# Kernel optimization log

Hardware: AMD Instinct MI355X
Metric: run time of the kernel (lower is better)

Reference implementation:

```python
import jax, jax.numpy as jnp
import numpy as np

T, B, IN, HID = 512, 64, 1024, 1024

def _linear_params(key, fan_in, fan_out):
    kw, kb = jax.random.split(key)
    bound = 1.0 / np.sqrt(fan_in)
    W = jax.random.uniform(kw, (fan_out, fan_in), jnp.float32, -bound, bound)
    b = jax.random.uniform(kb, (fan_out,), jnp.float32, -bound, bound)
    return W, b

def setup_inputs() -> dict:
    key = jax.random.key(0)
    ks = jax.random.split(key, 9)
    inp = {
        'inputs': jax.random.normal(ks[0], (T, B, IN), jnp.float32),
        'H0': jnp.zeros((B, HID), jnp.float32),
        'C0': jnp.zeros((B, HID), jnp.float32),
    }
    names = [('Wix','bix'),('Wih','bih'),('Wfx','bfx'),('Wfh','bfh'),
             ('Wox','box'),('Woh','boh'),('Wcx','bcx'),('Wch','bch')]
    fan_ins = [IN, HID, IN, HID, IN, HID, IN, HID]
    for (wn, bn), fi, k in zip(names, fan_ins, ks[1:]):
        W, b = _linear_params(k, fi, HID)
        inp[wn] = W
        inp[bn] = b
    return inp

def _lstm(inputs, H0, C0, Wix, bix, Wih, bih, Wfx, bfx, Wfh, bfh,
          Wox, box, Woh, boh, Wcx, bcx, Wch, bch):
    # Stack gate weights: order i, f, o, c_tilde
    Wx = jnp.concatenate([Wix, Wfx, Wox, Wcx], axis=0)      # [4H, IN]
    Wh = jnp.concatenate([Wih, Wfh, Woh, Wch], axis=0)      # [4H, H]
    bias = jnp.concatenate([bix + bih, bfx + bfh, box + boh, bcx + bch])  # [4H]
    # Precompute all input projections in one big GEMM: [T,B,4H]
    xproj = jnp.einsum('tbi,gi->tbg', inputs, Wx) + bias
    H = HID

    def step(carry, xg):
        h, c = carry
        g = xg + h @ Wh.T                                    # [B,4H]
        i = jax.nn.sigmoid(g[:, 0*H:1*H])
        f = jax.nn.sigmoid(g[:, 1*H:2*H])
        o = jax.nn.sigmoid(g[:, 2*H:3*H])
        ct = jnp.tanh(g[:, 3*H:4*H])
        c = f * c + i * ct
        h = o * jnp.tanh(c)
        return (h, c), h

    (Hf, Cf), outs = jax.lax.scan(step, (H0, C0), xproj)
    return outs, Hf, Cf

def reference(inputs, H0, C0, Wix, bix, Wih, bih, Wfx, bfx, Wfh, bfh,
              Wox, box, Woh, boh, Wcx, bcx, Wch, bch):
    return _lstm(inputs, H0, C0, Wix, bix, Wih, bih, Wfx, bfx, Wfh, bfh,
                 Wox, box, Woh, boh, Wcx, bcx, Wch, bch)
```

## Files before the change

### kernel.cpp

```cpp
#include <hip/hip_runtime.h>
#include <hip/hip_bf16.h>
#include <math.h>

#define T_STEPS 512
#define BATCH   64
#define INDIM   1024
#define HDIM    1024
#define NWG     128
#define NPROD   128
#define HSLOT   16384
#define XGSLOT  262144

using bf16x8 = __attribute__((ext_vector_type(8))) __bf16;
using f32x4  = __attribute__((ext_vector_type(4))) float;
typedef unsigned long long u64;

struct WP {
    const float* wx[4];
    const float* wh[4];
    const float* bx[4];
    const float* bh[4];
};

__global__ void pack_weights(WP p, __hip_bfloat16* __restrict__ Wx,
                             __hip_bfloat16* __restrict__ Wh, float* __restrict__ bias)
{
    int i = blockIdx.x * blockDim.x + threadIdx.x;
    const int stride = gridDim.x * blockDim.x;
    const int total = 4 * HDIM * INDIM;
    for (int idx = i; idx < total; idx += stride) {
        int g = idx >> 20;
        int r = idx & ((1 << 20) - 1);
        Wx[idx] = __float2bfloat16(p.wx[g][r]);
        Wh[idx] = __float2bfloat16(p.wh[g][r]);
    }
    if (i < 4 * HDIM) {
        int g = i >> 10, r = i & 1023;
        bias[i] = p.bx[g][r] + p.bh[g][r];
    }
}

__global__ void cast_pack(const float* __restrict__ in, u64* __restrict__ xbp)
{
    const int total = T_STEPS * BATCH * (INDIM / 8);
    int i = blockIdx.x * blockDim.x + threadIdx.x;
    const int stride = gridDim.x * blockDim.x;
    for (; i < total; i += stride) {
        const int t  = i >> 13;
        const int r  = i & 8191;
        const int b  = r >> 7;
        const int j  = (r & 127) << 3;
        const float* src = in + ((size_t)t << 16) + (b << 10) + j;
        float4 v0 = *reinterpret_cast<const float4*>(src);
        float4 v1 = *reinterpret_cast<const float4*>(src + 4);
        union { __hip_bfloat16 bh[8]; u64 q[2]; } u;
        u.bh[0] = __float2bfloat16(v0.x); u.bh[1] = __float2bfloat16(v0.y);
        u.bh[2] = __float2bfloat16(v0.z); u.bh[3] = __float2bfloat16(v0.w);
        u.bh[4] = __float2bfloat16(v1.x); u.bh[5] = __float2bfloat16(v1.y);
        u.bh[6] = __float2bfloat16(v1.z); u.bh[7] = __float2bfloat16(v1.w);
        const int wv = j >> 8, kk = (j >> 5) & 7, lhi = (j >> 3) & 3;
        const int m = b >> 4, rA = b & 15;
        const int lane = (lhi << 4) + rA;
        const int blk  = (((wv << 3) + kk) << 2) + m;
        u64* d = xbp + ((size_t)t << 14) + (size_t)blk * 128 + (lane << 1);
        d[0] = u.q[0];
        d[1] = u.q[1];
    }
}

__global__ void init_state(const float* __restrict__ H0, const float* __restrict__ C0,
                           __hip_bfloat16* __restrict__ hx, float* __restrict__ c)
{
    int i = blockIdx.x * blockDim.x + threadIdx.x;
    if (i < BATCH * HDIM) {
        int b = i >> 10, j = i & 1023;
        int m = b >> 4, rA = b & 15;
        int wv = j >> 8, kk = (j >> 5) & 7, lhi = (j >> 3) & 3, ii = j & 7;
        size_t idx = ((((size_t)(wv << 3) + kk) << 2) + m) * 512
                   + (((lhi << 4) + rA) << 3) + ii;
        hx[idx] = __float2bfloat16(H0[i]);
        c[i] = C0[i];
    }
}

__global__ void epilogue(const float* __restrict__ lasth, const float* __restrict__ c,
                         float* __restrict__ Hf, float* __restrict__ Cf)
{
    int i = blockIdx.x * blockDim.x + threadIdx.x;
    if (i < BATCH * HDIM) {
        Hf[i] = lasth[i];
        Cf[i] = c[i];
    }
}

__device__ __forceinline__ float fast_sigmoid(float x)
{
    return 1.f / (1.f + __expf(-x));
}
__device__ __forceinline__ float fast_tanh(float x)
{
    x = fminf(15.f, fmaxf(-15.f, x));
    const float e = __expf(2.f * x);
    return (e - 1.f) / (e + 1.f);
}

__global__ __launch_bounds__(256, 1) void lstm_persist(
    const u64* __restrict__ xbp,
    const __hip_bfloat16* __restrict__ Wx,
    const __hip_bfloat16* __restrict__ Wh,
    const float* __restrict__ bias,
    u64* __restrict__ hx,
    float* __restrict__ cbuf,
    float* __restrict__ out,
    unsigned* __restrict__ hflags,
    unsigned* __restrict__ xflags,
    float* __restrict__ xg)
{
    __shared__ float gl[4][64][33];
    __shared__ float hs[64][9];

    const int tid  = threadIdx.x;
    const int w    = tid >> 6;
    const int lane = tid & 63;
    const int rA   = lane & 15;
    const int kg   = (lane >> 4) << 3;
    const int bw   = blockIdx.x;

    if (bw >= NWG) {
        const int p   = bw - NWG;
        const int grp = p >> 5;
        const int pn  = p & 31;
        const int nb0 = pn << 7;

        for (int s = grp; s < T_STEPS; s += 4) {
            u64 aq[8][4][2];
#pragma unroll
            for (int kk = 0; kk < 8; ++kk)
#pragma unroll
                for (int m = 0; m < 4; ++m) {
                    const u64* q = xbp + ((size_t)s << 14)
                                 + ((((size_t)(w << 3) + kk) << 2) + m) * 128
                                 + (lane << 1);
                    aq[kk][m][0] = q[0];
                    aq[kk][m][1] = q[1];
                }

            if (s >= 8) {
                const unsigned need = (unsigned)(s - 7);
                const unsigned* f0 = hflags + lane * 16;
                const unsigned* f1 = hflags + (lane + 64) * 16;
                int guard = 1 << 18;
                while (--guard > 0) {
                    int ok = (__hip_atomic_load(f0, __ATOMIC_RELAXED, __HIP_MEMORY_SCOPE_AGENT) >= need) &&
                             (__hip_atomic_load(f1, __ATOMIC_RELAXED, __HIP_MEMORY_SCOPE_AGENT) >= need);
                    if (__all(ok)) break;
                    __builtin_amdgcn_s_sleep(1);
                }
            }

            float* xgs = xg + (size_t)(s & 7) * XGSLOT;
#pragma unroll 1
            for (int g32 = 0; g32 < 4; ++g32) {
                const int nb = nb0 + (g32 << 5);
                bf16x8 wxf[2][8];
#pragma unroll
                for (int n2 = 0; n2 < 2; ++n2) {
                    const __hip_bfloat16* xr =
                        Wx + (size_t)(nb + (n2 << 4) + rA) * 1024 + (w << 8) + kg;
#pragma unroll
                    for (int kk = 0; kk < 8; ++kk)
                        wxf[n2][kk] = *reinterpret_cast<const bf16x8*>(xr + (kk << 5));
                }
                f32x4 acc[2][4] = {};
#pragma unroll
                for (int kk = 0; kk < 8; ++kk)
#pragma unroll
                    for (int m = 0; m < 4; ++m) {
                        union { u64 q[2]; bf16x8 v; } c;
                        c.q[0] = aq[kk][m][0];
                        c.q[1] = aq[kk][m][1];
#pragma unroll
                        for (int n2 = 0; n2 < 2; ++n2)
                            acc[n2][m] = __builtin_amdgcn_mfma_f32_16x16x32_bf16(
                                c.v, wxf[n2][kk], acc[n2][m], 0, 0, 0);
                    }
#pragma unroll
                for (int n2 = 0; n2 < 2; ++n2)
#pragma unroll
                    for (int m = 0; m < 4; ++m) {
                        const int bb = (m << 4) + ((lane >> 4) << 2);
#pragma unroll
                        for (int r = 0; r < 4; ++r)
                            gl[w][bb + r][(n2 << 4) + rA] = acc[n2][m][r];
                    }
                __syncthreads();
                {
                    const int np = tid >> 3;
                    const int bb = (tid & 7) << 3;
                    union { float f[8]; u64 q[4]; } v;
#pragma unroll
                    for (int i = 0; i < 8; ++i)
                        v.f[i] = gl[0][bb + i][np] + gl[1][bb + i][np]
                               + gl[2][bb + i][np] + gl[3][bb + i][np];
                    u64* d = (u64*)(xgs + (size_t)(nb + np) * 64 + bb);
#pragma unroll
                    for (int q4 = 0; q4 < 4; ++q4)
                        __hip_atomic_store(d + q4, v.q[q4],
                                           __ATOMIC_RELAXED, __HIP_MEMORY_SCOPE_AGENT);
                }
                __syncthreads();
            }
            if (tid == 0)
                __hip_atomic_store(&xflags[p * 16], (unsigned)(s + 1),
                                   __ATOMIC_RELAXED, __HIP_MEMORY_SCOPE_AGENT);
        }
        return;
    }

    const int j0 = bw << 3;

    bf16x8 whf[2][8];
#pragma unroll
    for (int n2 = 0; n2 < 2; ++n2) {
        const int row  = (n2 << 4) + rA;
        const int grow = ((row >> 3) << 10) + j0 + (row & 7);
        const __hip_bfloat16* wr = Wh + ((size_t)grow << 10) + (w << 8) + kg;
#pragma unroll
        for (int kk = 0; kk < 8; ++kk)
            whf[n2][kk] = *reinterpret_cast<const bf16x8*>(wr + (kk << 5));
    }

    const int b = lane;
    float creg[2], brg[2][4];
#pragma unroll
    for (int e = 0; e < 2; ++e) {
        const int cl = (w << 1) + e;
        creg[e] = cbuf[(b << 10) + j0 + cl];
#pragma unroll
        for (int g = 0; g < 4; ++g) brg[e][g] = bias[(g << 10) + j0 + cl];
    }

    const int pblk = (((bw >> 5) << 3) + ((bw >> 2) & 7)) << 2;
    const unsigned gsto = (unsigned)(pblk + (b >> 4)) * 256
                        + (unsigned)((((bw & 3) << 4) + (b & 15)) << 2) + w;
    const unsigned* fq = hflags + (((w << 5) + (lane & 31)) << 4);

#define XV_FETCH(dst, ss)                                                      \
    do {                                                                       \
        const unsigned* fx_ = xflags +                                         \
            (((((unsigned)(ss) & 3) << 5) + (bw >> 4) + ((lane & 3) << 3)) << 4); \
        int guard_ = 1 << 18;                                                  \
        while (--guard_ > 0) {                                                 \
            unsigned v_ = __hip_atomic_load(fx_, __ATOMIC_RELAXED, __HIP_MEMORY_SCOPE_AGENT); \
            int ok_ = (lane < 4) ? (int)(v_ >= (unsigned)(ss) + 1) : 1;        \
            if (__all(ok_)) break;                                             \
            __builtin_amdgcn_s_sleep(1);                                       \
        }                                                                      \
        const float* xgs_ = xg + (size_t)((ss) & 7) * XGSLOT;                  \
        _Pragma("unroll") for (int e = 0; e < 2; ++e)                          \
        _Pragma("unroll") for (int g = 0; g < 4; ++g) {                        \
            unsigned uv_ = __hip_atomic_load(                                  \
                (const unsigned*)(xgs_ +                                       \
                    (size_t)((g << 10) + j0 + (w << 1) + e) * 64 + b),         \
                __ATOMIC_RELAXED, __HIP_MEMORY_SCOPE_AGENT);                   \
            dst[e][g] = __uint_as_float(uv_);                                  \
        }                                                                      \
    } while (0)

    float xv[2][4];
    XV_FETCH(xv, 0);

    for (int s = 0; s < T_STEPS; ++s) {
        const unsigned t = (unsigned)s;
        const u64* hp = hx + (size_t)(t & 3) * HSLOT;
        u64*       hn = hx + (size_t)((t + 1) & 3) * HSLOT;

        {
            int guard = 1 << 18;
            while (--guard > 0) {
                unsigned v = __hip_atomic_load(fq, __ATOMIC_RELAXED, __HIP_MEMORY_SCOPE_AGENT);
                if (__all((int)(v >= t))) break;
                __builtin_amdgcn_s_sleep(1);
            }
        }

        f32x4 acc[2][4] = {};
        {
            u64 aq[8][4][2];
#pragma unroll
            for (int kk = 0; kk < 8; ++kk)
#pragma unroll
                for (int m = 0; m < 4; ++m) {
                    const u64* q = hp + ((((size_t)(w << 3) + kk) << 2) + m) * 128
                                     + (lane << 1);
                    aq[kk][m][0] = __hip_atomic_load(q,     __ATOMIC_RELAXED, __HIP_MEMORY_SCOPE_AGENT);
                    aq[kk][m][1] = __hip_atomic_load(q + 1, __ATOMIC_RELAXED, __HIP_MEMORY_SCOPE_AGENT);
                }
            __builtin_amdgcn_sched_barrier(0);
#pragma unroll
            for (int kk = 0; kk < 8; ++kk)
#pragma unroll
                for (int m = 0; m < 4; ++m) {
                    union { u64 q[2]; bf16x8 v; } c;
                    c.q[0] = aq[kk][m][0];
                    c.q[1] = aq[kk][m][1];
#pragma unroll
                    for (int n2 = 0; n2 < 2; ++n2)
                        acc[n2][m] = __builtin_amdgcn_mfma_f32_16x16x32_bf16(
                            c.v, whf[n2][kk], acc[n2][m], 0, 0, 0);
                }
        }

#pragma unroll
        for (int n2 = 0; n2 < 2; ++n2)
#pragma unroll
            for (int m = 0; m < 4; ++m) {
                const int bb = (m << 4) + ((lane >> 4) << 2);
#pragma unroll
                for (int r = 0; r < 4; ++r)
                    gl[w][bb + r][(n2 << 4) + rA] = acc[n2][m][r];
            }
        __syncthreads();

        {
            float hv[2];
#pragma unroll
            for (int e = 0; e < 2; ++e) {
                const int cl = (w << 1) + e;
                float gv[4];
#pragma unroll
                for (int g = 0; g < 4; ++g)
                    gv[g] = gl[0][b][(g << 3) + cl] + gl[1][b][(g << 3) + cl]
                          + gl[2][b][(g << 3) + cl] + gl[3][b][(g << 3) + cl]
                          + brg[e][g] + xv[e][g];
                const float i_ = fast_sigmoid(gv[0]);
                const float f_ = fast_sigmoid(gv[1]);
                const float o_ = fast_sigmoid(gv[2]);
                const float ct = fast_tanh(gv[3]);
                const float cn = f_ * creg[e] + i_ * ct;
                creg[e] = cn;
                hv[e] = o_ * fast_tanh(cn);
                hs[b][cl] = hv[e];
            }
            union { __hip_bfloat16 bh[2]; unsigned u; } pk;
            pk.bh[0] = __float2bfloat16(hv[0]);
            pk.bh[1] = __float2bfloat16(hv[1]);
            __hip_atomic_store((unsigned*)hn + gsto, pk.u,
                               __ATOMIC_RELAXED, __HIP_MEMORY_SCOPE_AGENT);
        }
        __syncthreads();

        if (tid == 0)
            __hip_atomic_store(&hflags[bw * 16], t + 1,
                               __ATOMIC_RELAXED, __HIP_MEMORY_SCOPE_AGENT);

        if (s + 1 < T_STEPS) XV_FETCH(xv, s + 1);

        if (tid < 64) {
            float v[8];
#pragma unroll
            for (int k = 0; k < 8; ++k) v[k] = hs[tid][k];
            float* orow = out + (((size_t)s << 6) + tid) * 1024 + j0;
            *reinterpret_cast<float4*>(orow)     = make_float4(v[0], v[1], v[2], v[3]);
            *reinterpret_cast<float4*>(orow + 4) = make_float4(v[4], v[5], v[6], v[7]);
        }
    }

#pragma unroll
    for (int e = 0; e < 2; ++e)
        cbuf[(b << 10) + j0 + (w << 1) + e] = creg[e];
}

extern "C" void kernel_launch(void* const* d_in, const int* in_sizes, int n_in,
                              void* d_out, int out_size, void* d_ws, size_t ws_size,
                              hipStream_t stream)
{
    const float* inputs = (const float*)d_in[0];
    const float* H0     = (const float*)d_in[1];
    const float* C0     = (const float*)d_in[2];

    WP wp;
    wp.wx[0] = (const float*)d_in[3];  wp.bx[0] = (const float*)d_in[4];
    wp.wh[0] = (const float*)d_in[5];  wp.bh[0] = (const float*)d_in[6];
    wp.wx[1] = (const float*)d_in[7];  wp.bx[1] = (const float*)d_in[8];
    wp.wh[1] = (const float*)d_in[9];  wp.bh[1] = (const float*)d_in[10];
    wp.wx[2] = (const float*)d_in[11]; wp.bx[2] = (const float*)d_in[12];
    wp.wh[2] = (const float*)d_in[13]; wp.bh[2] = (const float*)d_in[14];
    wp.wx[3] = (const float*)d_in[15]; wp.bx[3] = (const float*)d_in[16];
    wp.wh[3] = (const float*)d_in[17]; wp.bh[3] = (const float*)d_in[18];

    char* ws = (char*)d_ws;
    size_t off = 0;
    auto alloc = [&](size_t bytes) {
        void* p = ws + off;
        off = (off + bytes + 255) & ~(size_t)255;
        return p;
    };
    __hip_bfloat16* Wx    = (__hip_bfloat16*)alloc((size_t)4 * HDIM * INDIM * 2);
    __hip_bfloat16* Wh    = (__hip_bfloat16*)alloc((size_t)4 * HDIM * HDIM * 2);
    float*          bias  = (float*)alloc((size_t)4 * HDIM * 4);
    u64*            xbp   = (u64*)alloc((size_t)T_STEPS * HSLOT * 8);
    u64*            hx    = (u64*)alloc((size_t)4 * HSLOT * 8);
    float*          cbuf  = (float*)alloc((size_t)BATCH * HDIM * 4);
    unsigned*       hflags= (unsigned*)alloc((size_t)NWG * 16 * 4);
    unsigned*       xflags= (unsigned*)alloc((size_t)NPROD * 16 * 4);
    float*          xg    = (float*)alloc((size_t)8 * XGSLOT * 4);
    if (off > ws_size) return;

    float* out = (float*)d_out;

    hipMemsetAsync(hflags, 0, (size_t)NWG * 16 * 4, stream);
    hipMemsetAsync(xflags, 0, (size_t)NPROD * 16 * 4, stream);
    hipLaunchKernelGGL(pack_weights, dim3(2048), dim3(256), 0, stream, wp, Wx, Wh, bias);
    hipLaunchKernelGGL(cast_pack, dim3(4096), dim3(256), 0, stream, inputs, xbp);
    hipLaunchKernelGGL(init_state, dim3(256), dim3(256), 0, stream,
                       H0, C0, (__hip_bfloat16*)hx, cbuf);

    hipLaunchKernelGGL(lstm_persist, dim3(NWG + NPROD), dim3(256), 0, stream,
                       (const u64*)xbp, (const __hip_bfloat16*)Wx,
                       (const __hip_bfloat16*)Wh, (const float*)bias,
                       hx, cbuf, out, hflags, xflags, xg);

    hipLaunchKernelGGL(epilogue, dim3(256), dim3(256), 0, stream,
                       out + (size_t)(T_STEPS - 1) * BATCH * HDIM, cbuf,
                       out + (size_t)T_STEPS * BATCH * HDIM,
                       out + (size_t)T_STEPS * BATCH * HDIM + BATCH * HDIM);
}
```

Measured before the change: 2.331 ms.

## Split batch into two independent recurrence chains to overlap gate math with GEMM

The persistent LSTM kernel now splits the 64-row batch into two 32-row chains, each with its own h ring buffer and flag array. Within each step the chain-A GEMM and gates run, then A's flag is published, then chain B runs, so other workgroups can start chain A of the next step while B is still finishing. This targets the serialized cross-workgroup wait-GEMM-gate latency on the recurrent critical path. In exchange it adds an extra flag wait, extra syncthreads, and smaller MFMA batches per GEMM.

```diff
diff --git a/kernel.cpp b/kernel.cpp
--- a/kernel.cpp
+++ b/kernel.cpp
@@ -8,7 +8,7 @@
 #define HDIM    1024
 #define NWG     128
 #define NPROD   128
-#define HSLOT   16384
+#define HSLOT2  8192
 #define XGSLOT  262144
 
 using bf16x8 = __attribute__((ext_vector_type(8))) __bf16;
@@ -74,9 +74,11 @@
     int i = blockIdx.x * blockDim.x + threadIdx.x;
     if (i < BATCH * HDIM) {
         int b = i >> 10, j = i & 1023;
-        int m = b >> 4, rA = b & 15;
+        int chain = b >> 5, bc = b & 31;
+        int m = bc >> 4, rA = bc & 15;
         int wv = j >> 8, kk = (j >> 5) & 7, lhi = (j >> 3) & 3, ii = j & 7;
-        size_t idx = ((((size_t)(wv << 3) + kk) << 2) + m) * 512
+        size_t idx = (size_t)chain * 4 * HSLOT2 * 4
+                   + ((((size_t)(wv << 3) + kk) << 1) + m) * 512
                    + (((lhi << 4) + rA) << 3) + ii;
         hx[idx] = __float2bfloat16(H0[i]);
         c[i] = C0[i];
@@ -112,7 +114,8 @@
     u64* __restrict__ hx,
     float* __restrict__ cbuf,
     float* __restrict__ out,
-    unsigned* __restrict__ hflags,
+    unsigned* __restrict__ hflagsA,
+    unsigned* __restrict__ hflagsB,
     unsigned* __restrict__ xflags,
     float* __restrict__ xg)
 {
@@ -147,8 +150,8 @@
 
             if (s >= 8) {
                 const unsigned need = (unsigned)(s - 7);
-                const unsigned* f0 = hflags + lane * 16;
-                const unsigned* f1 = hflags + (lane + 64) * 16;
+                const unsigned* f0 = hflagsB + lane * 16;
+                const unsigned* f1 = hflagsB + (lane + 64) * 16;
                 int guard = 1 << 18;
                 while (--guard > 0) {
                     int ok = (__hip_atomic_load(f0, __ATOMIC_RELAXED, __HIP_MEMORY_SCOPE_AGENT) >= need) &&
@@ -240,10 +243,14 @@
         for (int g = 0; g < 4; ++g) brg[e][g] = bias[(g << 10) + j0 + cl];
     }
 
-    const int pblk = (((bw >> 5) << 3) + ((bw >> 2) & 7)) << 2;
-    const unsigned gsto = (unsigned)(pblk + (b >> 4)) * 256
-                        + (unsigned)((((bw & 3) << 4) + (b & 15)) << 2) + w;
-    const unsigned* fq = hflags + (((w << 5) + (lane & 31)) << 4);
+    const int bc    = lane & 31;
+    const int pblk2 = (((bw >> 5) << 3) + ((bw >> 2) & 7)) << 1;
+    const unsigned gsto = (unsigned)(pblk2 + (bc >> 4)) * 256
+                        + (unsigned)((((bw & 3) << 4) + (bc & 15)) << 2) + w;
+    const unsigned* fqA = hflagsA + (((w << 5) + (lane & 31)) << 4);
+    const unsigned* fqB = hflagsB + (((w << 5) + (lane & 31)) << 4);
+    u64* const hcA = hx;
+    u64* const hcB = hx + 4 * HSLOT2;
 
 #define XV_FETCH(dst, ss)                                                      \
     do {                                                                       \
@@ -267,94 +274,107 @@
         }                                                                      \
     } while (0)
 
+#define CHAIN_GEMM(fq, hbase, t, acc)                                          \
+    do {                                                                       \
+        int guard_ = 1 << 18;                                                  \
+        while (--guard_ > 0) {                                                 \
+            unsigned v_ = __hip_atomic_load(fq, __ATOMIC_RELAXED, __HIP_MEMORY_SCOPE_AGENT); \
+            if (__all((int)(v_ >= (t)))) break;                                \
+            __builtin_amdgcn_s_sleep(1);                                       \
+        }                                                                      \
+        const u64* hp_ = (hbase) + (size_t)((t) & 3) * HSLOT2;                 \
+        u64 aq_[8][2][2];                                                      \
+        _Pragma("unroll") for (int kk = 0; kk < 8; ++kk)                       \
+        _Pragma("unroll") for (int m = 0; m < 2; ++m) {                        \
+            const u64* q_ = hp_ + ((((size_t)(w << 3) + kk) << 1) + m) * 128   \
+                               + (lane << 1);                                  \
+            aq_[kk][m][0] = __hip_atomic_load(q_,     __ATOMIC_RELAXED, __HIP_MEMORY_SCOPE_AGENT); \
+            aq_[kk][m][1] = __hip_atomic_load(q_ + 1, __ATOMIC_RELAXED, __HIP_MEMORY_SCOPE_AGENT); \
+        }                                                                      \
+        __builtin_amdgcn_sched_barrier(0);                                     \
+        _Pragma("unroll") for (int kk = 0; kk < 8; ++kk)                       \
+        _Pragma("unroll") for (int m = 0; m < 2; ++m) {                        \
+            union { u64 q[2]; bf16x8 v; } c_;                                  \
+            c_.q[0] = aq_[kk][m][0];                                           \
+            c_.q[1] = aq_[kk][m][1];                                           \
+            _Pragma("unroll") for (int n2 = 0; n2 < 2; ++n2)                   \
+                acc[n2][m] = __builtin_amdgcn_mfma_f32_16x16x32_bf16(          \
+                    c_.v, whf[n2][kk], acc[n2][m], 0, 0, 0);                   \
+        }                                                                      \
+    } while (0)
+
+#define GL_WRITE(acc, base)                                                    \
+    do {                                                                       \
+        _Pragma("unroll") for (int n2 = 0; n2 < 2; ++n2)                       \
+        _Pragma("unroll") for (int m = 0; m < 2; ++m) {                        \
+            const int bb = (base) + (m << 4) + ((lane >> 4) << 2);             \
+            _Pragma("unroll") for (int r = 0; r < 4; ++r)                      \
+                gl[w][bb + r][(n2 << 4) + rA] = acc[n2][m][r];                 \
+        }                                                                      \
+    } while (0)
+
+#define GATES(lo, hnp)                                                         \
+    do {                                                                       \
+        if ((lane & 32) == (lo)) {                                             \
+            float hv_[2];                                                      \
+            _Pragma("unroll") for (int e = 0; e < 2; ++e) {                    \
+                const int cl = (w << 1) + e;                                   \
+                float gv_[4];                                                  \
+                _Pragma("unroll") for (int g = 0; g < 4; ++g)                  \
+                    gv_[g] = gl[0][b][(g << 3) + cl] + gl[1][b][(g << 3) + cl] \
+                           + gl[2][b][(g << 3) + cl] + gl[3][b][(g << 3) + cl] \
+                           + brg[e][g] + xv[e][g];                             \
+                const float i_ = fast_sigmoid(gv_[0]);                         \
+                const float f_ = fast_sigmoid(gv_[1]);                         \
+                const float o_ = fast_sigmoid(gv_[2]);                         \
+                const float ct_ = fast_tanh(gv_[3]);                           \
+                const float cn_ = f_ * creg[e] + i_ * ct_;                     \
+                creg[e] = cn_;                                                 \
+                hv_[e] = o_ * fast_tanh(cn_);                                  \
+                hs[b][cl] = hv_[e];                                            \
+            }                                                                  \
+            union { __hip_bfloat16 bh[2]; unsigned u; } pk_;                   \
+            pk_.bh[0] = __float2bfloat16(hv_[0]);                              \
+            pk_.bh[1] = __float2bfloat16(hv_[1]);                              \
+            __hip_atomic_store((unsigned*)(hnp) + gsto, pk_.u,                 \
+                               __ATOMIC_RELAXED, __HIP_MEMORY_SCOPE_AGENT);    \
+        }                                                                      \
+    } while (0)
+
+
     float xv[2][4];
     XV_FETCH(xv, 0);
 
     for (int s = 0; s < T_STEPS; ++s) {
         const unsigned t = (unsigned)s;
-        const u64* hp = hx + (size_t)(t & 3) * HSLOT;
-        u64*       hn = hx + (size_t)((t + 1) & 3) * HSLOT;
+        u64* hnA = hcA + (size_t)((t + 1) & 3) * HSLOT2;
+        u64* hnB = hcB + (size_t)((t + 1) & 3) * HSLOT2;
 
         {
-            int guard = 1 << 18;
-            while (--guard > 0) {
-                unsigned v = __hip_atomic_load(fq, __ATOMIC_RELAXED, __HIP_MEMORY_SCOPE_AGENT);
-                if (__all((int)(v >= t))) break;
-                __builtin_amdgcn_s_sleep(1);
-            }
-        }
-
-        f32x4 acc[2][4] = {};
-        {
-            u64 aq[8][4][2];
-#pragma unroll
-            for (int kk = 0; kk < 8; ++kk)
-#pragma unroll
-                for (int m = 0; m < 4; ++m) {
-                    const u64* q = hp + ((((size_t)(w << 3) + kk) << 2) + m) * 128
-                                     + (lane << 1);
-                    aq[kk][m][0] = __hip_atomic_load(q,     __ATOMIC_RELAXED, __HIP_MEMORY_SCOPE_AGENT);
-                    aq[kk][m][1] = __hip_atomic_load(q + 1, __ATOMIC_RELAXED, __HIP_MEMORY_SCOPE_AGENT);
-                }
-            __builtin_amdgcn_sched_barrier(0);
-#pragma unroll
-            for (int kk = 0; kk < 8; ++kk)
-#pragma unroll
-                for (int m = 0; m < 4; ++m) {
-                    union { u64 q[2]; bf16x8 v; } c;
-                    c.q[0] = aq[kk][m][0];
-                    c.q[1] = aq[kk][m][1];
-#pragma unroll
-                    for (int n2 = 0; n2 < 2; ++n2)
-                        acc[n2][m] = __builtin_amdgcn_mfma_f32_16x16x32_bf16(
-                            c.v, whf[n2][kk], acc[n2][m], 0, 0, 0);
-                }
-        }
-
-#pragma unroll
-        for (int n2 = 0; n2 < 2; ++n2)
-#pragma unroll
-            for (int m = 0; m < 4; ++m) {
-                const int bb = (m << 4) + ((lane >> 4) << 2);
-#pragma unroll
-                for (int r = 0; r < 4; ++r)
-                    gl[w][bb + r][(n2 << 4) + rA] = acc[n2][m][r];
-            }
-        __syncthreads();
-
-        {
-            float hv[2];
-#pragma unroll
-            for (int e = 0; e < 2; ++e) {
-                const int cl = (w << 1) + e;
-                float gv[4];
-#pragma unroll
-                for (int g = 0; g < 4; ++g)
-                    gv[g] = gl[0][b][(g << 3) + cl] + gl[1][b][(g << 3) + cl]
-                          + gl[2][b][(g << 3) + cl] + gl[3][b][(g << 3) + cl]
-                          + brg[e][g] + xv[e][g];
-                const float i_ = fast_sigmoid(gv[0]);
-                const float f_ = fast_sigmoid(gv[1]);
-                const float o_ = fast_sigmoid(gv[2]);
-                const float ct = fast_tanh(gv[3]);
-                const float cn = f_ * creg[e] + i_ * ct;
-                creg[e] = cn;
-                hv[e] = o_ * fast_tanh(cn);
-                hs[b][cl] = hv[e];
-            }
-            union { __hip_bfloat16 bh[2]; unsigned u; } pk;
-            pk.bh[0] = __float2bfloat16(hv[0]);
-            pk.bh[1] = __float2bfloat16(hv[1]);
-            __hip_atomic_store((unsigned*)hn + gsto, pk.u,
-                               __ATOMIC_RELAXED, __HIP_MEMORY_SCOPE_AGENT);
+            f32x4 accA[2][2] = {};
+            CHAIN_GEMM(fqA, hcA, t, accA);
+            GL_WRITE(accA, 0);
         }
         __syncthreads();
-
+        GATES(0, hnA);
+
+        {
+            f32x4 accB[2][2] = {};
+            CHAIN_GEMM(fqB, hcB, t, accB);
+            GL_WRITE(accB, 32);
+        }
+        __syncthreads();
         if (tid == 0)
-            __hip_atomic_store(&hflags[bw * 16], t + 1,
+            __hip_atomic_store(&hflagsA[bw * 16], t + 1,
                                __ATOMIC_RELAXED, __HIP_MEMORY_SCOPE_AGENT);
+        GATES(32, hnB);
 
         if (s + 1 < T_STEPS) XV_FETCH(xv, s + 1);
+
+        __syncthreads();
+        if (tid == 0)
+            __hip_atomic_store(&hflagsB[bw * 16], t + 1,
+                               __ATOMIC_RELAXED, __HIP_MEMORY_SCOPE_AGENT);
 
         if (tid < 64) {
             float v[8];
@@ -396,20 +416,22 @@
         off = (off + bytes + 255) & ~(size_t)255;
         return p;
     };
-    __hip_bfloat16* Wx    = (__hip_bfloat16*)alloc((size_t)4 * HDIM * INDIM * 2);
-    __hip_bfloat16* Wh    = (__hip_bfloat16*)alloc((size_t)4 * HDIM * HDIM * 2);
-    float*          bias  = (float*)alloc((size_t)4 * HDIM * 4);
-    u64*            xbp   = (u64*)alloc((size_t)T_STEPS * HSLOT * 8);
-    u64*            hx    = (u64*)alloc((size_t)4 * HSLOT * 8);
-    float*          cbuf  = (float*)alloc((size_t)BATCH * HDIM * 4);
-    unsigned*       hflags= (unsigned*)alloc((size_t)NWG * 16 * 4);
-    unsigned*       xflags= (unsigned*)alloc((size_t)NPROD * 16 * 4);
-    float*          xg    = (float*)alloc((size_t)8 * XGSLOT * 4);
+    __hip_bfloat16* Wx     = (__hip_bfloat16*)alloc((size_t)4 * HDIM * INDIM * 2);
+    __hip_bfloat16* Wh     = (__hip_bfloat16*)alloc((size_t)4 * HDIM * HDIM * 2);
+    float*          bias   = (float*)alloc((size_t)4 * HDIM * 4);
+    u64*            xbp    = (u64*)alloc((size_t)T_STEPS * 16384 * 8);
+    u64*            hx     = (u64*)alloc((size_t)2 * 4 * HSLOT2 * 8);
+    float*          cbuf   = (float*)alloc((size_t)BATCH * HDIM * 4);
+    unsigned*       hflagsA= (unsigned*)alloc((size_t)NWG * 16 * 4);
+    unsigned*       hflagsB= (unsigned*)alloc((size_t)NWG * 16 * 4);
+    unsigned*       xflags = (unsigned*)alloc((size_t)NPROD * 16 * 4);
+    float*          xg     = (float*)alloc((size_t)8 * XGSLOT * 4);
     if (off > ws_size) return;
 
     float* out = (float*)d_out;
 
-    hipMemsetAsync(hflags, 0, (size_t)NWG * 16 * 4, stream);
+    hipMemsetAsync(hflagsA, 0, (size_t)NWG * 16 * 4, stream);
+    hipMemsetAsync(hflagsB, 0, (size_t)NWG * 16 * 4, stream);
     hipMemsetAsync(xflags, 0, (size_t)NPROD * 16 * 4, stream);
     hipLaunchKernelGGL(pack_weights, dim3(2048), dim3(256), 0, stream, wp, Wx, Wh, bias);
     hipLaunchKernelGGL(cast_pack, dim3(4096), dim3(256), 0, stream, inputs, xbp);
@@ -419,7 +441,7 @@
     hipLaunchKernelGGL(lstm_persist, dim3(NWG + NPROD), dim3(256), 0, stream,
                        (const u64*)xbp, (const __hip_bfloat16*)Wx,
                        (const __hip_bfloat16*)Wh, (const float*)bias,
-                       hx, cbuf, out, hflags, xflags, xg);
+                       hx, cbuf, out, hflagsA, hflagsB, xflags, xg);
 
     hipLaunchKernelGGL(epilogue, dim3(256), dim3(256), 0, stream,
                        out + (size_t)(T_STEPS - 1) * BATCH * HDIM, cbuf,
```

Result: slower. 3.043 ms (+30.5%).
